# Performance work log

Hardware: AMD Instinct MI355X
Metric: run time of the kernel (lower is better)

## Reference

```python
import jax, jax.numpy as jnp
import numpy as np

N = 4096          # patch_dim**2, patch_dim=64
F_IN = 44         # pre_Nfeat = Nfeat/3
F_OUT = 44
K = 16            # min_nn - 8
RANK = 11         # rank_theta


def setup_inputs() -> dict:
    key = jax.random.key(0)
    ks = jax.random.split(key, 6)
    return {
        "h": jax.random.normal(ks[0], (1, N, F_IN), jnp.float32),
        "local_mask": jnp.ones((N, N), jnp.float32),
        "W_lab": jax.random.normal(ks[1], (F_IN, F_IN), jnp.float32) * (1.0 / np.sqrt(F_IN)),
        "b_lab": jax.random.normal(ks[2], (1, F_IN), jnp.float32) * 0.1,
        "W_th1": jax.random.normal(ks[3], (F_IN, F_IN * RANK), jnp.float32) * (1.0 / F_IN),
        "b_th1": jnp.zeros((1, RANK, F_IN), jnp.float32),
        "W_th2": jax.random.normal(ks[4], (F_IN, F_OUT * RANK), jnp.float32) * (1.0 / F_IN),
        "b_th2": jnp.zeros((1, RANK, F_OUT), jnp.float32),
        "W_thl": jax.random.normal(ks[5], (F_IN, RANK), jnp.float32) * (1.0 / np.sqrt(RANK)),
        "b_thl": jnp.zeros((1, RANK), jnp.float32),
    }


def reference(h, local_mask, W_lab, b_lab, W_th1, b_th1, W_th2, b_th2, W_thl, b_thl):
    # --- compute_graph: pairwise sq. distances, masked, self-dist forced minimal ---
    hh = h[0]                                        # [N, F]
    hg = jax.lax.stop_gradient(hh)                   # torch detaches h for the graph
    sq = jnp.sum(hg * hg, axis=-1)                   # [N]
    D = jnp.abs(sq[:, None] + sq[None, :] - 2.0 * (hg @ hg.T))
    D = D * local_mask - 2.0 * jnp.eye(N, dtype=D.dtype)
    # --- kNN: 25 smallest distances; keep ranks 9..24 as neighbors, rank 0 = self ---
    _, top_idx = jax.lax.top_k(-D, K + 9)            # [N, 25]
    nbr_idx = top_idx[:, 9:].reshape(-1)             # [N*K] node-major edge order
    ctr_idx = jnp.repeat(top_idx[:, 0], K)           # [N*K]
    # --- gather (irregular access, the kernel target) ---
    x_tilde1 = hh[nbr_idx]                           # [E, F] neighbor features
    x_tilde2 = hh[ctr_idx]                           # [E, F] center features
    labels = x_tilde1 - x_tilde2                     # [E, F]
    d_labels = jnp.sum(labels * labels, axis=-1).reshape(N, K)
    # --- edge-conditioned low-rank filter generation ---
    lab = jax.nn.leaky_relu(labels @ W_lab + b_lab, negative_slope=0.2)  # [E, F]
    theta1 = (lab @ W_th1).reshape(-1, RANK, F_IN) + b_th1               # [E, R, F]
    theta2 = (lab @ W_th2).reshape(-1, RANK, F_OUT) + b_th2              # [E, R, Fo]
    thetal = lab @ W_thl + b_thl                                         # [E, R]
    t = jnp.einsum('erf,ef->er', theta1, x_tilde1) * thetal              # [E, R]
    x = jnp.einsum('erf,er->ef', theta2, t)                              # [E, Fo]
    # --- distance-weighted mean over K neighbors (scatter-mean) ---
    x = x.reshape(N, K, F_OUT) * jnp.exp(-d_labels / 10.0)[:, :, None]
    x = jnp.mean(x, axis=1)
    return x.reshape(1, N, F_OUT)
```

## Files before the change

### kernel.cpp

```cpp
#include <hip/hip_runtime.h>
#include <float.h>

#define N 4096
#define FI 44
#define RK 11
#define KNN 16
#define NSEL 25
#define NROW 4
#define ME 496

typedef unsigned long long u64;
typedef unsigned int u32;

__global__ __launch_bounds__(256) void k_prep_all(const float* __restrict__ h,
                                                  float* __restrict__ sq,
                                                  float* __restrict__ hT,
                                                  const float* __restrict__ W1,
                                                  const float* __restrict__ b1,
                                                  const float* __restrict__ W2,
                                                  const float* __restrict__ b2,
                                                  float* __restrict__ P1e,
                                                  float* __restrict__ W2T4) {
  const int tid = threadIdx.x;
  if (blockIdx.x < 16) {
    int n = blockIdx.x * 256 + tid;
    const float4* hr = reinterpret_cast<const float4*>(h + (size_t)n * FI);
    float v[FI];
    float s = 0.f;
#pragma unroll
    for (int c4 = 0; c4 < 11; c4++) {
      float4 x = hr[c4];
      v[4*c4] = x.x; v[4*c4+1] = x.y; v[4*c4+2] = x.z; v[4*c4+3] = x.w;
      s += x.x*x.x + x.y*x.y + x.z*x.z + x.w*x.w;
    }
    sq[n] = s;
#pragma unroll
    for (int c = 0; c < FI; c++) hT[c * N + n] = v[c];
  } else if (blockIdx.x < 272) {
    const int grp = tid >> 6, lane = tid & 63;
    const int nb = (blockIdx.x - 16) * 16 + grp * 4;
    const float4* h4 = reinterpret_cast<const float4*>(h);
    float4 hq[4][11];
#pragma unroll
    for (int q = 0; q < 4; q++)
#pragma unroll
      for (int c4 = 0; c4 < 11; c4++)
        hq[q][c4] = h4[(size_t)(nb + q) * 11 + c4];
#pragma unroll
    for (int i = 0; i < 8; i++) {
      int m = lane + 64 * i;
      if (m < 495) {
        const float4* wrow = reinterpret_cast<const float4*>(
            (m < 484) ? W1 + (size_t)(m % FI) * 484 + (m / FI) * FI
                      : b1 + (size_t)(m - 484) * FI);
        float a0 = 0.f, a1 = 0.f, a2 = 0.f, a3 = 0.f;
#pragma unroll
        for (int c4 = 0; c4 < 11; c4++) {
          float4 wv = wrow[c4];
          a0 += wv.x*hq[0][c4].x + wv.y*hq[0][c4].y + wv.z*hq[0][c4].z + wv.w*hq[0][c4].w;
          a1 += wv.x*hq[1][c4].x + wv.y*hq[1][c4].y + wv.z*hq[1][c4].z + wv.w*hq[1][c4].w;
          a2 += wv.x*hq[2][c4].x + wv.y*hq[2][c4].y + wv.z*hq[2][c4].z + wv.w*hq[2][c4].w;
          a3 += wv.x*hq[3][c4].x + wv.y*hq[3][c4].y + wv.z*hq[3][c4].z + wv.w*hq[3][c4].w;
        }
        P1e[(size_t)(nb + 0) * ME + m] = a0;
        P1e[(size_t)(nb + 1) * ME + m] = a1;
        P1e[(size_t)(nb + 2) * ME + m] = a2;
        P1e[(size_t)(nb + 3) * ME + m] = a3;
      }
    }
  } else {
    int idx0 = (blockIdx.x - 272) * 256 + tid;
    for (int idx = idx0; idx < 496 * 64; idx += 16 * 256) {
      int mc = idx >> 8;
      int fo = (idx >> 2) & 63;
      int i  = idx & 3;
      int m  = 4 * mc + i;
      float v = 0.f;
      if (fo < FI && m < 495) {
        if (m < 484) { int c = m % FI, r = m / FI; v = W2[c * 484 + r * FI + fo]; }
        else         { v = b2[(m - 484) * FI + fo]; }
      }
      W2T4[idx] = v;
    }
  }
}

__global__ __launch_bounds__(512) void k_dist_sweep(const float* __restrict__ hT,
                                                    const float* __restrict__ sq,
                                                    const float* __restrict__ mask,
                                                    int* __restrict__ gcnt,
                                                    u64* __restrict__ gcand) {
  __shared__ __align__(16) float hi[NROW][FI];
  __shared__ float sqi[NROW];
  __shared__ u32 lmin[NROW][512];
  __shared__ u32 Tsh[NROW];
  __shared__ int cnts[NROW];
  __shared__ u64 cbuf[NROW][128];
  const int tid = threadIdx.x;
  const int rowgrp = blockIdx.x >> 1;
  const int half = blockIdx.x & 1;
  const int r0 = rowgrp * NROW;
  const int w = tid >> 6, lane = tid & 63;
  const int cb = half * 512 + tid;
  const int jb = 4 * cb;

  if (tid < NROW) { cnts[tid] = 0; sqi[tid] = sq[r0 + tid]; }
  for (int t = tid; t < NROW * FI; t += 512) {
    int rr = t / FI, c = t % FI;
    hi[rr][c] = hT[c * N + (r0 + rr)];
  }
  __syncthreads();

  const float4* hT4 = reinterpret_cast<const float4*>(hT);
  const float4* sq4p = reinterpret_cast<const float4*>(sq);
  const float4* mask4 = reinterpret_cast<const float4*>(mask);

  float4 sq4 = sq4p[cb];
  float4 m4r[NROW];
#pragma unroll
  for (int rr = 0; rr < NROW; rr++)
    m4r[rr] = mask4[(size_t)(r0 + rr) * 1024 + cb];

  float4 acc[NROW];
#pragma unroll
  for (int rr = 0; rr < NROW; rr++) acc[rr] = make_float4(0.f, 0.f, 0.f, 0.f);
#pragma unroll 4
  for (int c = 0; c < FI; c++) {
    float4 v = hT4[(size_t)c * 1024 + cb];
#pragma unroll
    for (int rr = 0; rr < NROW; rr++) {
      float hc = hi[rr][c];
      acc[rr].x += hc * v.x; acc[rr].y += hc * v.y;
      acc[rr].z += hc * v.z; acc[rr].w += hc * v.w;
    }
  }

  u32 key[NROW][4];
#pragma unroll
  for (int rr = 0; rr < NROW; rr++) {
    int row = r0 + rr;
    float sqr = sqi[rr];
    float d0 = fabsf(sqr + sq4.x - 2.f * acc[rr].x) * m4r[rr].x;
    float d1 = fabsf(sqr + sq4.y - 2.f * acc[rr].y) * m4r[rr].y;
    float d2 = fabsf(sqr + sq4.z - 2.f * acc[rr].z) * m4r[rr].z;
    float d3 = fabsf(sqr + sq4.w - 2.f * acc[rr].w) * m4r[rr].w;
    d0 -= (jb + 0 == row) ? 2.f : 0.f;
    d1 -= (jb + 1 == row) ? 2.f : 0.f;
    d2 -= (jb + 2 == row) ? 2.f : 0.f;
    d3 -= (jb + 3 == row) ? 2.f : 0.f;
    u32 u0 = __float_as_uint(d0); u0 ^= (u32)((int)u0 >> 31) | 0x80000000u;
    u32 u1 = __float_as_uint(d1); u1 ^= (u32)((int)u1 >> 31) | 0x80000000u;
    u32 u2 = __float_as_uint(d2); u2 ^= (u32)((int)u2 >> 31) | 0x80000000u;
    u32 u3 = __float_as_uint(d3); u3 ^= (u32)((int)u3 >> 31) | 0x80000000u;
    key[rr][0] = u0; key[rr][1] = u1; key[rr][2] = u2; key[rr][3] = u3;
  }

#pragma unroll
  for (int rr = 0; rr < NROW; rr++) {
    u32 m01 = key[rr][0] < key[rr][1] ? key[rr][0] : key[rr][1];
    u32 m23 = key[rr][2] < key[rr][3] ? key[rr][2] : key[rr][3];
    lmin[rr][tid] = m01 < m23 ? m01 : m23;
  }
  __syncthreads();

  if (w < NROW) {
    u32 g = lmin[w][lane];
#pragma unroll
    for (int k = 1; k < 8; k++) {
      u32 x = lmin[w][64 * k + lane];
      g = x < g ? x : g;
    }
#pragma unroll
    for (int kk = 2; kk <= 64; kk <<= 1)
#pragma unroll
      for (int jj = kk >> 1; jj > 0; jj >>= 1) {
        u32 o = __shfl_xor(g, jj, 64);
        bool low = (lane & jj) == 0, asc = (lane & kk) == 0;
        u32 mn = o < g ? o : g, mx = o < g ? g : o;
        g = (low == asc) ? mn : mx;
      }
    if (lane == 24) Tsh[w] = g;
  }
  __syncthreads();

#pragma unroll
  for (int rr = 0; rr < NROW; rr++) {
    u32 Tr = Tsh[rr];
#pragma unroll
    for (int i = 0; i < 4; i++) {
      if (key[rr][i] <= Tr) {
        int p = atomicAdd(&cnts[rr], 1);
        if (p < 128) cbuf[rr][p] = ((u64)key[rr][i] << 12) | (u64)(jb + i);
      }
    }
  }
  __syncthreads();

  if (w < NROW) {
    int row = r0 + w;
    int cw = cnts[w]; if (cw > 128) cw = 128;
    int base = 0;
    if (lane == 0) base = atomicAdd(&gcnt[row], cw);
    base = __shfl(base, 0, 64);
    for (int i = lane; i < cw; i += 64) {
      int dst = base + i;
      if (dst < 128) gcand[(size_t)row * 128 + dst] = cbuf[w][i];
    }
  }
}

__global__ __launch_bounds__(512) void k_sort(const int* __restrict__ gcnt,
                                              const u64* __restrict__ gcand,
                                              int* __restrict__ ctr_idx,
                                              int* __restrict__ nbr_idx) {
  const int tid = threadIdx.x;
  const int w = tid >> 6, lane = tid & 63;
  const int row = blockIdx.x * 8 + w;
  int cnt = gcnt[row]; if (cnt > 128) cnt = 128;
  const u64 UMAX = ~0ull;
  u64 v0 = (lane < cnt) ? gcand[(size_t)row * 128 + lane] : UMAX;
  u64 v1 = (64 + lane < cnt) ? gcand[(size_t)row * 128 + 64 + lane] : UMAX;
#pragma unroll
  for (int kk = 2; kk <= 128; kk <<= 1) {
#pragma unroll
    for (int jj = kk >> 1; jj > 0; jj >>= 1) {
      if (jj >= 64) {
        bool asc = (lane & kk) == 0;
        u64 mn = v0 < v1 ? v0 : v1, mx = v0 < v1 ? v1 : v0;
        v0 = asc ? mn : mx; v1 = asc ? mx : mn;
      } else {
        bool low = (lane & jj) == 0;
        bool asc0 = (lane & kk) == 0;
        bool asc1 = ((64 + lane) & kk) == 0;
        u64 o0 = __shfl_xor(v0, jj, 64);
        v0 = (low == asc0) ? (o0 < v0 ? o0 : v0) : (o0 < v0 ? v0 : o0);
        u64 o1 = __shfl_xor(v1, jj, 64);
        v1 = (low == asc1) ? (o1 < v1 ? o1 : v1) : (o1 < v1 ? v1 : o1);
      }
    }
  }
  int idx = (int)(v0 & 4095ull);
  if (lane == 0) ctr_idx[row] = idx;
  if (lane >= 9 && lane < NSEL) nbr_idx[row * KNN + (lane - 9)] = idx;
}

__global__ __launch_bounds__(256) void k_edge_out(
    const float* __restrict__ h,
    const int* __restrict__ ctr_idx, const int* __restrict__ nbr_idx,
    const float* __restrict__ W_lab, const float* __restrict__ b_lab,
    const float* __restrict__ Wl, const float* __restrict__ bl,
    const float* __restrict__ P1e,
    const float* __restrict__ W2T4,
    float* __restrict__ out)
{
  __shared__ __align__(16) float WlabT[FI][FI];
  __shared__ __align__(16) float lbl[64][FI];
  __shared__ __align__(16) float WlT[RK][FI];
  __shared__ __align__(16) float hcs[4][FI];
  __shared__ __align__(16) float GeL[4][ME];
  __shared__ __align__(16) float pacc[4][4][64];
  __shared__ float blabS[FI];
  __shared__ float blS[RK];
  __shared__ float tfs[64][12];
  __shared__ float wexpS[64];
  __shared__ int nbrL[64];
  __shared__ int ctrL[4];
  const int tid = threadIdx.x;
  const int b = blockIdx.x;
  const float4* h4 = reinterpret_cast<const float4*>(h);

  if (tid < 64) nbrL[tid] = nbr_idx[b * 64 + tid];
  if (tid < 4) ctrL[tid] = ctr_idx[b * 4 + tid];
  if (tid < RK) blS[tid] = bl[tid];
  if (tid >= 64 && tid < 64 + FI) blabS[tid - 64] = b_lab[tid - 64];
  for (int t = tid; t < FI * FI; t += 256) {
    int c = t / FI, f = t % FI;
    WlabT[f][c] = W_lab[t];
  }
  for (int t = tid; t < FI * RK; t += 256) {
    int c = t / RK, r = t % RK;
    WlT[r][c] = Wl[t];
  }
  __syncthreads();

  if (tid < 44) {
    int nn = tid / 11, c4 = tid % 11;
    *reinterpret_cast<float4*>(&hcs[nn][4 * c4]) = h4[(size_t)ctrL[nn] * 11 + c4];
  }
  __syncthreads();
  for (int t = tid; t < 64 * 11; t += 256) {
    int e = t / 11, c4 = t % 11;
    float4 hv = h4[(size_t)nbrL[e] * 11 + c4];
    float4 hc = *reinterpret_cast<const float4*>(&hcs[e >> 4][4 * c4]);
    float4 d;
    d.x = hv.x - hc.x; d.y = hv.y - hc.y; d.z = hv.z - hc.z; d.w = hv.w - hc.w;
    *reinterpret_cast<float4*>(&lbl[e][4 * c4]) = d;
  }
  __syncthreads();

  const int e = tid >> 2;
  const int g = tid & 3;

  float4 lbr[11];
#pragma unroll
  for (int c4 = 0; c4 < 11; c4++)
    lbr[c4] = *reinterpret_cast<const float4*>(&lbl[e][4 * c4]);
  if (g == 0) {
    float s = 0.f;
#pragma unroll
    for (int c4 = 0; c4 < 11; c4++)
      s += lbr[c4].x*lbr[c4].x + lbr[c4].y*lbr[c4].y + lbr[c4].z*lbr[c4].z + lbr[c4].w*lbr[c4].w;
    wexpS[e] = expf(-s * 0.1f) * (1.0f / 16.0f);
  }

  float la[11];
#pragma unroll
  for (int u = 0; u < 11; u++) {
    int f = g + 4 * u;
    float acc = blabS[f];
#pragma unroll
    for (int c4 = 0; c4 < 11; c4++) {
      float4 wv = *reinterpret_cast<const float4*>(&WlabT[f][4 * c4]);
      acc += wv.x*lbr[c4].x + wv.y*lbr[c4].y + wv.z*lbr[c4].z + wv.w*lbr[c4].w;
    }
    la[u] = acc >= 0.f ? acc : 0.2f * acc;
  }
  __syncthreads();
#pragma unroll
  for (int u = 0; u < 11; u++) lbl[e][g + 4 * u] = la[u];
  __syncthreads();

  {
#pragma unroll
    for (int c4 = 0; c4 < 11; c4++)
      lbr[c4] = *reinterpret_cast<const float4*>(&lbl[e][4 * c4]);
    const float* P1r = P1e + (size_t)nbrL[e] * ME;
    float wex = wexpS[e];
#pragma unroll
    for (int rr = 0; rr < 3; rr++) {
      int r = g + 4 * rr;
      if (r < RK) {
        float tp = 0.f, tlp = 0.f;
#pragma unroll
        for (int c4 = 0; c4 < 11; c4++) {
          float4 p4 = *reinterpret_cast<const float4*>(P1r + r * FI + 4 * c4);
          float4 w4 = *reinterpret_cast<const float4*>(&WlT[r][4 * c4]);
          float4 l4 = lbr[c4];
          tp  += l4.x*p4.x + l4.y*p4.y + l4.z*p4.z + l4.w*p4.w;
          tlp += l4.x*w4.x + l4.y*w4.y + l4.z*w4.z + l4.w*w4.w;
        }
        tfs[e][r] = (tp + P1r[484 + r]) * (tlp + blS[r]) * wex;
      }
    }
  }
  __syncthreads();

  const int nn = tid >> 6, lane = tid & 63;
  const int w = nn;
  if (lane < FI) {
    float acc2[RK];
#pragma unroll
    for (int r = 0; r < RK; r++) acc2[r] = 0.f;
    for (int k = 0; k < KNN; k++) {
      float lv = lbl[nn * 16 + k][lane];
#pragma unroll
      for (int r = 0; r < RK; r++) acc2[r] += lv * tfs[nn * 16 + k][r];
    }
#pragma unroll
    for (int r = 0; r < RK; r++) GeL[nn][r * FI + lane] = acc2[r];
  } else if (lane < FI + RK) {
    int r = lane - FI;
    float ss = 0.f;
    for (int k = 0; k < KNN; k++) ss += tfs[nn * 16 + k][r];
    GeL[nn][484 + r] = ss;
  } else if (lane == 55) {
    GeL[nn][495] = 0.f;
  }
  __syncthreads();

  {
    const float4* W2v = reinterpret_cast<const float4*>(W2T4);
    float a0 = 0.f, a1 = 0.f, a2 = 0.f, a3 = 0.f;
    for (int mc = w * 31; mc < (w + 1) * 31; mc++) {
      float4 wv = W2v[mc * 64 + lane];
      float4 g0 = *reinterpret_cast<const float4*>(&GeL[0][4 * mc]);
      float4 g1 = *reinterpret_cast<const float4*>(&GeL[1][4 * mc]);
      float4 g2 = *reinterpret_cast<const float4*>(&GeL[2][4 * mc]);
      float4 g3 = *reinterpret_cast<const float4*>(&GeL[3][4 * mc]);
      a0 += wv.x*g0.x + wv.y*g0.y + wv.z*g0.z + wv.w*g0.w;
      a1 += wv.x*g1.x + wv.y*g1.y + wv.z*g1.z + wv.w*g1.w;
      a2 += wv.x*g2.x + wv.y*g2.y + wv.z*g2.z + wv.w*g2.w;
      a3 += wv.x*g3.x + wv.y*g3.y + wv.z*g3.z + wv.w*g3.w;
    }
    pacc[w][0][lane] = a0;
    pacc[w][1][lane] = a1;
    pacc[w][2][lane] = a2;
    pacc[w][3][lane] = a3;
  }
  __syncthreads();

  if (tid < 4 * FI) {
    int n2 = tid / FI, fo = tid - (tid / FI) * FI;
    out[(size_t)(b * 4 + n2) * FI + fo] =
        pacc[0][n2][fo] + pacc[1][n2][fo] + pacc[2][n2][fo] + pacc[3][n2][fo];
  }
}

extern "C" void kernel_launch(void* const* d_in, const int* in_sizes, int n_in,
                              void* d_out, int out_size, void* d_ws, size_t ws_size,
                              hipStream_t stream) {
  const float* h     = (const float*)d_in[0];
  const float* mask  = (const float*)d_in[1];
  const float* W_lab = (const float*)d_in[2];
  const float* b_lab = (const float*)d_in[3];
  const float* W1    = (const float*)d_in[4];
  const float* b1    = (const float*)d_in[5];
  const float* W2    = (const float*)d_in[6];
  const float* b2    = (const float*)d_in[7];
  const float* Wl    = (const float*)d_in[8];
  const float* bl    = (const float*)d_in[9];

  u64*   gcand = (u64*)d_ws;
  int*   gcnt  = (int*)(gcand + (size_t)N * 128);
  float* sqw   = (float*)(gcnt + N);
  float* hT    = sqw + N;
  int*   ctr   = (int*)(hT + (size_t)FI * N);
  int*   nbr   = ctr + N;
  float* P1e   = (float*)(nbr + N * KNN);
  float* W2T4  = P1e + (size_t)N * ME;

  hipMemsetAsync(gcnt, 0, N * sizeof(int), stream);
  k_prep_all<<<288, 256, 0, stream>>>(h, sqw, hT, W1, b1, W2, b2, P1e, W2T4);
  k_dist_sweep<<<2 * (N / NROW), 512, 0, stream>>>(hT, sqw, mask, gcnt, gcand);
  k_sort<<<N / 8, 512, 0, stream>>>(gcnt, gcand, ctr, nbr);
  k_edge_out<<<N * KNN / 64, 256, 0, stream>>>(h, ctr, nbr, W_lab, b_lab, Wl, bl, P1e, W2T4, (float*)d_out);
}
```

Measured before the change: 105.2 us.

## Fuse kNN sort into edge kernel, fold memset into prep, double rows per sweep block

Removes the separate sort kernel and the memset launch. The gcnt zeroing moves into the prep kernel and the per-row bitonic sort of candidates runs at the start of the edge-output kernel, so neighbor indices are no longer written to and read back from global memory. The distance sweep now handles 8 rows per block instead of 4, halving grid size and reusing each hT load across more rows. It recomputes distance keys in a second pass instead of keeping them in registers, streaming the mask per row, and relaxes the threshold by 64 ulps, which trades extra ALU work and mask reads for lower register pressure.

```diff
diff --git a/kernel.cpp b/kernel.cpp
--- a/kernel.cpp
+++ b/kernel.cpp
@@ -6,7 +6,7 @@
 #define RK 11
 #define KNN 16
 #define NSEL 25
-#define NROW 4
+#define NROW 8
 #define ME 496
 
 typedef unsigned long long u64;
@@ -20,10 +20,12 @@
                                                   const float* __restrict__ W2,
                                                   const float* __restrict__ b2,
                                                   float* __restrict__ P1e,
-                                                  float* __restrict__ W2T4) {
+                                                  float* __restrict__ W2T4,
+                                                  int* __restrict__ gcnt) {
   const int tid = threadIdx.x;
   if (blockIdx.x < 16) {
     int n = blockIdx.x * 256 + tid;
+    gcnt[n] = 0;
     const float4* hr = reinterpret_cast<const float4*>(h + (size_t)n * FI);
     float v[FI];
     float s = 0.f;
@@ -115,12 +117,6 @@
   const float4* sq4p = reinterpret_cast<const float4*>(sq);
   const float4* mask4 = reinterpret_cast<const float4*>(mask);
 
-  float4 sq4 = sq4p[cb];
-  float4 m4r[NROW];
-#pragma unroll
-  for (int rr = 0; rr < NROW; rr++)
-    m4r[rr] = mask4[(size_t)(r0 + rr) * 1024 + cb];
-
   float4 acc[NROW];
 #pragma unroll
   for (int rr = 0; rr < NROW; rr++) acc[rr] = make_float4(0.f, 0.f, 0.f, 0.f);
@@ -135,35 +131,36 @@
     }
   }
 
-  u32 key[NROW][4];
-#pragma unroll
-  for (int rr = 0; rr < NROW; rr++) {
-    int row = r0 + rr;
-    float sqr = sqi[rr];
-    float d0 = fabsf(sqr + sq4.x - 2.f * acc[rr].x) * m4r[rr].x;
-    float d1 = fabsf(sqr + sq4.y - 2.f * acc[rr].y) * m4r[rr].y;
-    float d2 = fabsf(sqr + sq4.z - 2.f * acc[rr].z) * m4r[rr].z;
-    float d3 = fabsf(sqr + sq4.w - 2.f * acc[rr].w) * m4r[rr].w;
-    d0 -= (jb + 0 == row) ? 2.f : 0.f;
-    d1 -= (jb + 1 == row) ? 2.f : 0.f;
-    d2 -= (jb + 2 == row) ? 2.f : 0.f;
-    d3 -= (jb + 3 == row) ? 2.f : 0.f;
-    u32 u0 = __float_as_uint(d0); u0 ^= (u32)((int)u0 >> 31) | 0x80000000u;
-    u32 u1 = __float_as_uint(d1); u1 ^= (u32)((int)u1 >> 31) | 0x80000000u;
-    u32 u2 = __float_as_uint(d2); u2 ^= (u32)((int)u2 >> 31) | 0x80000000u;
-    u32 u3 = __float_as_uint(d3); u3 ^= (u32)((int)u3 >> 31) | 0x80000000u;
-    key[rr][0] = u0; key[rr][1] = u1; key[rr][2] = u2; key[rr][3] = u3;
-  }
-
-#pragma unroll
-  for (int rr = 0; rr < NROW; rr++) {
-    u32 m01 = key[rr][0] < key[rr][1] ? key[rr][0] : key[rr][1];
-    u32 m23 = key[rr][2] < key[rr][3] ? key[rr][2] : key[rr][3];
-    lmin[rr][tid] = m01 < m23 ? m01 : m23;
-  }
-  __syncthreads();
-
-  if (w < NROW) {
+  const float4 sq4 = sq4p[cb];
+
+  {
+    float4 mcur = mask4[(size_t)r0 * 1024 + cb];
+#pragma unroll 1
+    for (int rr = 0; rr < NROW; rr++) {
+      float4 m4 = mcur;
+      if (rr < NROW - 1) mcur = mask4[(size_t)(r0 + rr + 1) * 1024 + cb];
+      int row = r0 + rr;
+      float sqr = sqi[rr];
+      float d0 = fabsf(sqr + sq4.x - 2.f * acc[rr].x) * m4.x;
+      float d1 = fabsf(sqr + sq4.y - 2.f * acc[rr].y) * m4.y;
+      float d2 = fabsf(sqr + sq4.z - 2.f * acc[rr].z) * m4.z;
+      float d3 = fabsf(sqr + sq4.w - 2.f * acc[rr].w) * m4.w;
+      if (jb + 0 == row) d0 -= 2.f;
+      if (jb + 1 == row) d1 -= 2.f;
+      if (jb + 2 == row) d2 -= 2.f;
+      if (jb + 3 == row) d3 -= 2.f;
+      u32 u0 = __float_as_uint(d0); u0 ^= (u32)((int)u0 >> 31) | 0x80000000u;
+      u32 u1 = __float_as_uint(d1); u1 ^= (u32)((int)u1 >> 31) | 0x80000000u;
+      u32 u2 = __float_as_uint(d2); u2 ^= (u32)((int)u2 >> 31) | 0x80000000u;
+      u32 u3 = __float_as_uint(d3); u3 ^= (u32)((int)u3 >> 31) | 0x80000000u;
+      u32 m01 = u0 < u1 ? u0 : u1;
+      u32 m23 = u2 < u3 ? u2 : u3;
+      lmin[rr][tid] = m01 < m23 ? m01 : m23;
+    }
+  }
+  __syncthreads();
+
+  {
     u32 g = lmin[w][lane];
 #pragma unroll
     for (int k = 1; k < 8; k++) {
@@ -183,20 +180,37 @@
   }
   __syncthreads();
 
-#pragma unroll
-  for (int rr = 0; rr < NROW; rr++) {
-    u32 Tr = Tsh[rr];
-#pragma unroll
-    for (int i = 0; i < 4; i++) {
-      if (key[rr][i] <= Tr) {
-        int p = atomicAdd(&cnts[rr], 1);
-        if (p < 128) cbuf[rr][p] = ((u64)key[rr][i] << 12) | (u64)(jb + i);
-      }
-    }
-  }
-  __syncthreads();
-
-  if (w < NROW) {
+  {
+    float4 mcur = mask4[(size_t)r0 * 1024 + cb];
+#pragma unroll 1
+    for (int rr = 0; rr < NROW; rr++) {
+      float4 m4 = mcur;
+      if (rr < NROW - 1) mcur = mask4[(size_t)(r0 + rr + 1) * 1024 + cb];
+      int row = r0 + rr;
+      float sqr = sqi[rr];
+      float d0 = fabsf(sqr + sq4.x - 2.f * acc[rr].x) * m4.x;
+      float d1 = fabsf(sqr + sq4.y - 2.f * acc[rr].y) * m4.y;
+      float d2 = fabsf(sqr + sq4.z - 2.f * acc[rr].z) * m4.z;
+      float d3 = fabsf(sqr + sq4.w - 2.f * acc[rr].w) * m4.w;
+      if (jb + 0 == row) d0 -= 2.f;
+      if (jb + 1 == row) d1 -= 2.f;
+      if (jb + 2 == row) d2 -= 2.f;
+      if (jb + 3 == row) d3 -= 2.f;
+      u32 u0 = __float_as_uint(d0); u0 ^= (u32)((int)u0 >> 31) | 0x80000000u;
+      u32 u1 = __float_as_uint(d1); u1 ^= (u32)((int)u1 >> 31) | 0x80000000u;
+      u32 u2 = __float_as_uint(d2); u2 ^= (u32)((int)u2 >> 31) | 0x80000000u;
+      u32 u3 = __float_as_uint(d3); u3 ^= (u32)((int)u3 >> 31) | 0x80000000u;
+      u32 Tr = Tsh[rr];
+      u32 Tp = (Tr > 0xFFFFFFBFu) ? 0xFFFFFFFFu : Tr + 64u;
+      if (u0 <= Tp) { int p = atomicAdd(&cnts[rr], 1); if (p < 128) cbuf[rr][p] = ((u64)u0 << 12) | (u64)(jb + 0); }
+      if (u1 <= Tp) { int p = atomicAdd(&cnts[rr], 1); if (p < 128) cbuf[rr][p] = ((u64)u1 << 12) | (u64)(jb + 1); }
+      if (u2 <= Tp) { int p = atomicAdd(&cnts[rr], 1); if (p < 128) cbuf[rr][p] = ((u64)u2 << 12) | (u64)(jb + 2); }
+      if (u3 <= Tp) { int p = atomicAdd(&cnts[rr], 1); if (p < 128) cbuf[rr][p] = ((u64)u3 << 12) | (u64)(jb + 3); }
+    }
+  }
+  __syncthreads();
+
+  {
     int row = r0 + w;
     int cw = cnts[w]; if (cw > 128) cw = 128;
     int base = 0;
@@ -209,44 +223,9 @@
   }
 }
 
-__global__ __launch_bounds__(512) void k_sort(const int* __restrict__ gcnt,
-                                              const u64* __restrict__ gcand,
-                                              int* __restrict__ ctr_idx,
-                                              int* __restrict__ nbr_idx) {
-  const int tid = threadIdx.x;
-  const int w = tid >> 6, lane = tid & 63;
-  const int row = blockIdx.x * 8 + w;
-  int cnt = gcnt[row]; if (cnt > 128) cnt = 128;
-  const u64 UMAX = ~0ull;
-  u64 v0 = (lane < cnt) ? gcand[(size_t)row * 128 + lane] : UMAX;
-  u64 v1 = (64 + lane < cnt) ? gcand[(size_t)row * 128 + 64 + lane] : UMAX;
-#pragma unroll
-  for (int kk = 2; kk <= 128; kk <<= 1) {
-#pragma unroll
-    for (int jj = kk >> 1; jj > 0; jj >>= 1) {
-      if (jj >= 64) {
-        bool asc = (lane & kk) == 0;
-        u64 mn = v0 < v1 ? v0 : v1, mx = v0 < v1 ? v1 : v0;
-        v0 = asc ? mn : mx; v1 = asc ? mx : mn;
-      } else {
-        bool low = (lane & jj) == 0;
-        bool asc0 = (lane & kk) == 0;
-        bool asc1 = ((64 + lane) & kk) == 0;
-        u64 o0 = __shfl_xor(v0, jj, 64);
-        v0 = (low == asc0) ? (o0 < v0 ? o0 : v0) : (o0 < v0 ? v0 : o0);
-        u64 o1 = __shfl_xor(v1, jj, 64);
-        v1 = (low == asc1) ? (o1 < v1 ? o1 : v1) : (o1 < v1 ? v1 : o1);
-      }
-    }
-  }
-  int idx = (int)(v0 & 4095ull);
-  if (lane == 0) ctr_idx[row] = idx;
-  if (lane >= 9 && lane < NSEL) nbr_idx[row * KNN + (lane - 9)] = idx;
-}
-
 __global__ __launch_bounds__(256) void k_edge_out(
     const float* __restrict__ h,
-    const int* __restrict__ ctr_idx, const int* __restrict__ nbr_idx,
+    const int* __restrict__ gcnt, const u64* __restrict__ gcand,
     const float* __restrict__ W_lab, const float* __restrict__ b_lab,
     const float* __restrict__ Wl, const float* __restrict__ bl,
     const float* __restrict__ P1e,
@@ -269,8 +248,6 @@
   const int b = blockIdx.x;
   const float4* h4 = reinterpret_cast<const float4*>(h);
 
-  if (tid < 64) nbrL[tid] = nbr_idx[b * 64 + tid];
-  if (tid < 4) ctrL[tid] = ctr_idx[b * 4 + tid];
   if (tid < RK) blS[tid] = bl[tid];
   if (tid >= 64 && tid < 64 + FI) blabS[tid - 64] = b_lab[tid - 64];
   for (int t = tid; t < FI * FI; t += 256) {
@@ -280,6 +257,37 @@
   for (int t = tid; t < FI * RK; t += 256) {
     int c = t / RK, r = t % RK;
     WlT[r][c] = Wl[t];
+  }
+
+  {
+    const int nn = tid >> 6, lane = tid & 63;
+    const int row = b * 4 + nn;
+    int cnt = gcnt[row]; if (cnt > 128) cnt = 128;
+    const u64 UMAX = ~0ull;
+    u64 v0 = (lane < cnt) ? gcand[(size_t)row * 128 + lane] : UMAX;
+    u64 v1 = (64 + lane < cnt) ? gcand[(size_t)row * 128 + 64 + lane] : UMAX;
+#pragma unroll
+    for (int kk = 2; kk <= 128; kk <<= 1) {
+#pragma unroll
+      for (int jj = kk >> 1; jj > 0; jj >>= 1) {
+        if (jj >= 64) {
+          bool asc = (lane & kk) == 0;
+          u64 mn = v0 < v1 ? v0 : v1, mx = v0 < v1 ? v1 : v0;
+          v0 = asc ? mn : mx; v1 = asc ? mx : mn;
+        } else {
+          bool low = (lane & jj) == 0;
+          bool asc0 = (lane & kk) == 0;
+          bool asc1 = ((64 + lane) & kk) == 0;
+          u64 o0 = __shfl_xor(v0, jj, 64);
+          v0 = (low == asc0) ? (o0 < v0 ? o0 : v0) : (o0 < v0 ? v0 : o0);
+          u64 o1 = __shfl_xor(v1, jj, 64);
+          v1 = (low == asc1) ? (o1 < v1 ? o1 : v1) : (o1 < v1 ? v1 : o1);
+        }
+      }
+    }
+    int idx = (int)(v0 & 4095ull);
+    if (lane == 0) ctrL[nn] = idx;
+    if (lane >= 9 && lane < NSEL) nbrL[nn * 16 + (lane - 9)] = idx;
   }
   __syncthreads();
 
@@ -424,14 +432,10 @@
   int*   gcnt  = (int*)(gcand + (size_t)N * 128);
   float* sqw   = (float*)(gcnt + N);
   float* hT    = sqw + N;
-  int*   ctr   = (int*)(hT + (size_t)FI * N);
-  int*   nbr   = ctr + N;
-  float* P1e   = (float*)(nbr + N * KNN);
+  float* P1e   = hT + (size_t)FI * N;
   float* W2T4  = P1e + (size_t)N * ME;
 
-  hipMemsetAsync(gcnt, 0, N * sizeof(int), stream);
-  k_prep_all<<<288, 256, 0, stream>>>(h, sqw, hT, W1, b1, W2, b2, P1e, W2T4);
+  k_prep_all<<<288, 256, 0, stream>>>(h, sqw, hT, W1, b1, W2, b2, P1e, W2T4, gcnt);
   k_dist_sweep<<<2 * (N / NROW), 512, 0, stream>>>(hT, sqw, mask, gcnt, gcand);
-  k_sort<<<N / 8, 512, 0, stream>>>(gcnt, gcand, ctr, nbr);
-  k_edge_out<<<N * KNN / 64, 256, 0, stream>>>(h, ctr, nbr, W_lab, b_lab, Wl, bl, P1e, W2T4, (float*)d_out);
+  k_edge_out<<<N / 4, 256, 0, stream>>>(h, gcnt, gcand, W_lab, b_lab, Wl, bl, P1e, W2T4, (float*)d_out);
 }
```

Measured after the change: 132.3 us. 1.26x slower.
